# Optimization experiments

Measured on AMD Instinct MI355X. Metric: run time of the kernel, lower is better.

## Reference

```python
import jax, jax.numpy as jnp
import numpy as np

# Module config (matches init_kwargs)
T, B, C = 2048, 8, 1024   # seq_len, batch, input_size
H, K = 16, 31             # num_heads, kernel_size
PAD_L = 30                # padding_l (causal)


def setup_inputs() -> dict:
    key = jax.random.key(0)
    k1, k2 = jax.random.split(key)
    x = jax.random.normal(k1, (T, B, C), dtype=jnp.float32)
    # nn.Parameter(num_heads, kernel_size), xavier-init approximated by randn
    weight = jax.random.normal(k2, (H, K), dtype=jnp.float32)
    return {"x": x, "weight": weight}


def reference(x, weight):
    # x: (T, B, C); weight: (H, K)
    # weight_softmax=True: softmax over kernel taps per head
    w = jax.nn.softmax(weight, axis=-1)  # (H, K)
    # permute to (B, C, T) as the CUDA kernel expects
    x_bct = jnp.transpose(x, (1, 2, 0))
    # expand per-head kernel to per-channel depthwise kernel: (C, 1, K)
    w_ck = jnp.repeat(w, C // H, axis=0)[:, None, :]
    # lightconv: out[b,c,t] = sum_k w[head(c),k] * x_pad[b,c,t+k],
    # left pad = PAD_L, right pad = K-1-PAD_L (causal when PAD_L=K-1).
    # conv_general_dilated is cross-correlation, matching the CUDA kernel.
    out = jax.lax.conv_general_dilated(
        x_bct, w_ck,
        window_strides=(1,),
        padding=[(PAD_L, K - 1 - PAD_L)],
        dimension_numbers=("NCH", "OIH", "NCH"),
        feature_group_count=C,
    )  # (B, C, T)
    # bias=False, so just permute back to (T, B, C)
    return jnp.transpose(out, (2, 0, 1))
```

## Files before the change

kernel.cpp:

```cpp
#include <hip/hip_runtime.h>
#include <math.h>

#define T_LEN 2048
#define B_SZ  8
#define C_SZ  1024
#define NH    16
#define KW    31
#define HALO  (KW - 1)
#define TT    8
#define CHUNK 64
#define NTILE (CHUNK / TT)
#define RING  32
#define WIN   (TT + HALO)
#define ROWSTRIDE (B_SZ * C_SZ)

#define GLOBAL_AS(p) ((const __attribute__((address_space(1))) void*)(p))
#define LDS_AS(p)    ((__attribute__((address_space(3))) void*)(p))

__global__ __launch_bounds__(64, 4) void lightconv_kernel(
    const float* __restrict__ x, const float* __restrict__ weight,
    float* __restrict__ out) {
  __shared__ float ring[RING][64];
  const int lane = threadIdx.x;

  const int cgrp = blockIdx.x & 15;
  const int tc   = blockIdx.x >> 4;
  const int b    = blockIdx.y;
  const int c0   = cgrp * 64;
  const int tb   = tc * CHUNK;

  float wv[KW];
  float m = -1e30f;
#pragma unroll
  for (int k = 0; k < KW; ++k) {
    wv[k] = weight[cgrp * KW + k];
    m = fmaxf(m, wv[k]);
  }
  float s = 0.f;
#pragma unroll
  for (int k = 0; k < KW; ++k) {
    wv[k] = expf(wv[k] - m);
    s += wv[k];
  }
  const float inv = 1.f / s;
  float wk[KW];
#pragma unroll
  for (int k = 0; k < KW; ++k) {
    wk[k] = __uint_as_float(
        __builtin_amdgcn_readfirstlane(__float_as_uint(wv[k] * inv)));
  }

  const float* xbase = x + (size_t)b * C_SZ + c0;
  const int lane_off = (lane >> 4) * ROWSTRIDE + (lane & 15) * 4;

  float xv[WIN];
  if (tb == 0) {
#pragma unroll
    for (int i = 0; i < HALO; ++i) xv[i] = 0.f;
  } else {
#pragma unroll
    for (int i = 0; i < HALO; ++i) {
      xv[i] = xbase[(size_t)(tb - HALO + i) * ROWSTRIDE + lane];
    }
  }
#pragma unroll
  for (int r4 = 0; r4 < 4; ++r4) {
    const float* gp = xbase + (size_t)(tb + 4 * r4) * ROWSTRIDE + lane_off;
    __builtin_amdgcn_global_load_lds(GLOBAL_AS(gp), LDS_AS(&ring[4 * r4][0]),
                                     16, 0, 0);
  }

#pragma unroll
  for (int j = 0; j < NTILE; ++j) {
    const int tstart = tb + j * TT;

    if (j <= NTILE - 3) {
#pragma unroll
      for (int r4 = 0; r4 < 2; ++r4) {
        const float* gp =
            xbase + (size_t)(tstart + 2 * TT + 4 * r4) * ROWSTRIDE + lane_off;
        __builtin_amdgcn_global_load_lds(
            GLOBAL_AS(gp), LDS_AS(&ring[(8 * j + 16 + 4 * r4) & (RING - 1)][0]),
            16, 0, 0);
      }
    }
    if (j == 0)                asm volatile("s_waitcnt vmcnt(4)"  ::: "memory");
    else if (j == 1)           asm volatile("s_waitcnt vmcnt(12)" ::: "memory");
    else if (j == NTILE - 2)   asm volatile("s_waitcnt vmcnt(18)" ::: "memory");
    else if (j == NTILE - 1)   asm volatile("s_waitcnt vmcnt(16)" ::: "memory");
    else                       asm volatile("s_waitcnt vmcnt(20)" ::: "memory");
    __builtin_amdgcn_sched_barrier(0);

#pragma unroll
    for (int i = 0; i < TT; ++i) {
      xv[HALO + i] = ring[(8 * j + i) & (RING - 1)][lane];
    }
    float* op = out + ((size_t)tstart * B_SZ + b) * C_SZ + c0 + lane;
#pragma unroll
    for (int o = 0; o < TT; ++o) {
      float a = 0.f;
#pragma unroll
      for (int k = 0; k < KW; ++k) a = fmaf(wk[k], xv[o + k], a);
      op[(size_t)o * ROWSTRIDE] = a;
    }
#pragma unroll
    for (int i = 0; i < HALO; ++i) xv[i] = xv[i + TT];
  }
}

extern "C" void kernel_launch(void* const* d_in, const int* in_sizes, int n_in,
                              void* d_out, int out_size, void* d_ws, size_t ws_size,
                              hipStream_t stream) {
  const float* x = (const float*)d_in[0];
  const float* w = (const float*)d_in[1];
  float* out = (float*)d_out;
  (void)in_sizes; (void)n_in; (void)out_size; (void)d_ws; (void)ws_size;

  dim3 grid((C_SZ / 64) * (T_LEN / CHUNK), B_SZ);
  dim3 block(64);
  lightconv_kernel<<<grid, block, 0, stream>>>(x, w, out);
}
```

Baseline: 33.14 us.

## Process two channels per lane with float2 loads and 128-channel blocks

Each 64-lane block now covers 128 channels, so every lane handles two adjacent channels through float2 halo loads, LDS reads and stores. The grid is halved and per-lane work doubles. Weights now vary per half-wave, since each block spans two heads, so the readfirstlane broadcast into scalar registers is dropped and the 31 taps sit in vector registers. This doubles the register window, which is why occupancy is lowered to 3 and the vmcnt waits are retuned for the extra async loads.

```diff
diff --git a/kernel.cpp b/kernel.cpp
--- a/kernel.cpp
+++ b/kernel.cpp
@@ -12,28 +12,30 @@
 #define NTILE (CHUNK / TT)
 #define RING  32
 #define WIN   (TT + HALO)
+#define CGW   128
 #define ROWSTRIDE (B_SZ * C_SZ)
 
 #define GLOBAL_AS(p) ((const __attribute__((address_space(1))) void*)(p))
 #define LDS_AS(p)    ((__attribute__((address_space(3))) void*)(p))
 
-__global__ __launch_bounds__(64, 4) void lightconv_kernel(
+__global__ __launch_bounds__(64, 3) void lightconv_kernel(
     const float* __restrict__ x, const float* __restrict__ weight,
     float* __restrict__ out) {
-  __shared__ float ring[RING][64];
+  __shared__ float ring[RING][CGW];
   const int lane = threadIdx.x;
 
-  const int cgrp = blockIdx.x & 15;
-  const int tc   = blockIdx.x >> 4;
+  const int cgrp = blockIdx.x & 7;
+  const int tc   = blockIdx.x >> 3;
   const int b    = blockIdx.y;
-  const int c0   = cgrp * 64;
+  const int c0   = cgrp * CGW;
   const int tb   = tc * CHUNK;
 
+  const int head = cgrp * 2 + (lane >> 5);
   float wv[KW];
   float m = -1e30f;
 #pragma unroll
   for (int k = 0; k < KW; ++k) {
-    wv[k] = weight[cgrp * KW + k];
+    wv[k] = weight[head * KW + k];
     m = fmaxf(m, wv[k]);
   }
   float s = 0.f;
@@ -45,28 +47,26 @@
   const float inv = 1.f / s;
   float wk[KW];
 #pragma unroll
-  for (int k = 0; k < KW; ++k) {
-    wk[k] = __uint_as_float(
-        __builtin_amdgcn_readfirstlane(__float_as_uint(wv[k] * inv)));
-  }
+  for (int k = 0; k < KW; ++k) wk[k] = wv[k] * inv;
 
   const float* xbase = x + (size_t)b * C_SZ + c0;
-  const int lane_off = (lane >> 4) * ROWSTRIDE + (lane & 15) * 4;
+  const float* xch   = xbase + 2 * lane;
+  const int lane_off = (lane >> 5) * ROWSTRIDE + (lane & 31) * 4;
 
-  float xv[WIN];
+  float2 xv[WIN];
   if (tb == 0) {
 #pragma unroll
-    for (int i = 0; i < HALO; ++i) xv[i] = 0.f;
+    for (int i = 0; i < HALO; ++i) xv[i] = make_float2(0.f, 0.f);
   } else {
 #pragma unroll
     for (int i = 0; i < HALO; ++i) {
-      xv[i] = xbase[(size_t)(tb - HALO + i) * ROWSTRIDE + lane];
+      xv[i] = *(const float2*)&xch[(size_t)(tb - HALO + i) * ROWSTRIDE];
     }
   }
 #pragma unroll
-  for (int r4 = 0; r4 < 4; ++r4) {
-    const float* gp = xbase + (size_t)(tb + 4 * r4) * ROWSTRIDE + lane_off;
-    __builtin_amdgcn_global_load_lds(GLOBAL_AS(gp), LDS_AS(&ring[4 * r4][0]),
+  for (int r2 = 0; r2 < 8; ++r2) {
+    const float* gp = xbase + (size_t)(tb + 2 * r2) * ROWSTRIDE + lane_off;
+    __builtin_amdgcn_global_load_lds(GLOBAL_AS(gp), LDS_AS(&ring[2 * r2][0]),
                                      16, 0, 0);
   }
 
@@ -76,32 +76,36 @@
 
     if (j <= NTILE - 3) {
 #pragma unroll
-      for (int r4 = 0; r4 < 2; ++r4) {
+      for (int r2 = 0; r2 < 4; ++r2) {
         const float* gp =
-            xbase + (size_t)(tstart + 2 * TT + 4 * r4) * ROWSTRIDE + lane_off;
+            xbase + (size_t)(tstart + 2 * TT + 2 * r2) * ROWSTRIDE + lane_off;
         __builtin_amdgcn_global_load_lds(
-            GLOBAL_AS(gp), LDS_AS(&ring[(8 * j + 16 + 4 * r4) & (RING - 1)][0]),
+            GLOBAL_AS(gp), LDS_AS(&ring[(8 * j + 16 + 2 * r2) & (RING - 1)][0]),
             16, 0, 0);
       }
     }
-    if (j == 0)                asm volatile("s_waitcnt vmcnt(4)"  ::: "memory");
-    else if (j == 1)           asm volatile("s_waitcnt vmcnt(12)" ::: "memory");
-    else if (j == NTILE - 2)   asm volatile("s_waitcnt vmcnt(18)" ::: "memory");
+    if (j == 0)                asm volatile("s_waitcnt vmcnt(8)"  ::: "memory");
+    else if (j == 1)           asm volatile("s_waitcnt vmcnt(16)" ::: "memory");
+    else if (j == NTILE - 2)   asm volatile("s_waitcnt vmcnt(20)" ::: "memory");
     else if (j == NTILE - 1)   asm volatile("s_waitcnt vmcnt(16)" ::: "memory");
-    else                       asm volatile("s_waitcnt vmcnt(20)" ::: "memory");
+    else                       asm volatile("s_waitcnt vmcnt(24)" ::: "memory");
     __builtin_amdgcn_sched_barrier(0);
 
 #pragma unroll
     for (int i = 0; i < TT; ++i) {
-      xv[HALO + i] = ring[(8 * j + i) & (RING - 1)][lane];
+      const float2* rp = (const float2*)&ring[(8 * j + i) & (RING - 1)][0];
+      xv[HALO + i] = rp[lane];
     }
-    float* op = out + ((size_t)tstart * B_SZ + b) * C_SZ + c0 + lane;
+    float* opb = out + ((size_t)tstart * B_SZ + b) * C_SZ + c0 + 2 * lane;
 #pragma unroll
     for (int o = 0; o < TT; ++o) {
-      float a = 0.f;
+      float ax = 0.f, ay = 0.f;
 #pragma unroll
-      for (int k = 0; k < KW; ++k) a = fmaf(wk[k], xv[o + k], a);
-      op[(size_t)o * ROWSTRIDE] = a;
+      for (int k = 0; k < KW; ++k) {
+        ax = fmaf(wk[k], xv[o + k].x, ax);
+        ay = fmaf(wk[k], xv[o + k].y, ay);
+      }
+      *(float2*)&opb[(size_t)o * ROWSTRIDE] = make_float2(ax, ay);
     }
 #pragma unroll
     for (int i = 0; i < HALO; ++i) xv[i] = xv[i + TT];
@@ -116,7 +120,7 @@
   float* out = (float*)d_out;
   (void)in_sizes; (void)n_in; (void)out_size; (void)d_ws; (void)ws_size;
 
-  dim3 grid((C_SZ / 64) * (T_LEN / CHUNK), B_SZ);
+  dim3 grid((C_SZ / CGW) * (T_LEN / CHUNK), B_SZ);
   dim3 block(64);
   lightconv_kernel<<<grid, block, 0, stream>>>(x, w, out);
 }
```

Measured after the change: 30.27 us, median of 2. 8.7% less time.
